# Performance work log

Hardware: AMD Instinct MI355X
Metric: run time of the kernel (lower is better)

## Reference

```python
import jax, jax.numpy as jnp
import numpy as np

B, FEAT, HID, LAT, NQ, NEMB = 2048, 840, 256, 128, 12, 512


def setup_inputs() -> dict:
    key = jax.random.key(0)
    ks = jax.random.split(key, 6)
    return {
        "x": jax.random.normal(ks[0], (B, FEAT), jnp.float32),
        "w1": jax.random.normal(ks[1], (HID, 1, 3), jnp.float32) * 0.1,   # Conv1d(1->256, k=3)
        "b1": jnp.zeros((HID,), jnp.float32),
        "w2": jax.random.normal(ks[2], (LAT, HID, 3), jnp.float32) * 0.05,  # Conv1d(256->128, k=3)
        "b2": jnp.zeros((LAT,), jnp.float32),
        # 12 codebooks of (512, 128), init uniform(-1/n_emb, 1/n_emb) per the torch code
        "codebooks": jax.random.uniform(ks[3], (NQ, NEMB, LAT), jnp.float32, -1.0 / NEMB, 1.0 / NEMB),
    }


def _encode(x, w1, b1, w2, b2):
    # x: (B, FEAT) -> unsqueeze channel dim -> NCW conv stack -> adaptive avg pool(1)
    h = x[:, None, :]  # (B, 1, FEAT)
    h = jax.lax.conv_general_dilated(h, w1, (1,), 'SAME',
                                     dimension_numbers=('NCH', 'OIH', 'NCH'))
    h = jax.nn.relu(h + b1[None, :, None])
    h = jax.lax.conv_general_dilated(h, w2, (1,), 'SAME',
                                     dimension_numbers=('NCH', 'OIH', 'NCH'))
    h = jax.nn.relu(h + b2[None, :, None])
    return h.mean(axis=2)  # AdaptiveAvgPool1d(1) + squeeze -> (B, LAT)


def _rvq(z_flat, codebooks):
    # sequential residual VQ: 12 stages of cdist -> argmin -> gather -> residual update
    def step(residual, cb):
        # squared L2 distances: ||r||^2 - 2 r C^T + ||c||^2, shape (B, NEMB)
        d = (jnp.sum(residual ** 2, axis=1, keepdims=True)
             - 2.0 * (residual @ cb.T)
             + jnp.sum(cb ** 2, axis=1)[None, :])
        idx = jnp.argmin(d, axis=1)          # (B,)
        q = cb[idx]                          # (B, LAT) embedding gather
        residual = residual - jax.lax.stop_gradient(q)  # .detach() in torch
        return residual, (q, idx)

    _, (qs, idxs) = jax.lax.scan(step, z_flat, codebooks)  # qs: (NQ, B, LAT)
    return qs.sum(axis=0), idxs.T  # (B, LAT), (B, NQ)


def reference(x, w1, b1, w2, b2, codebooks):
    z = _encode(x, w1, b1, w2, b2)            # (B, LAT)
    zq, idx = _rvq(z, codebooks)              # L = 1 so flat == (B, LAT)
    return zq[:, None, :], idx[:, None, :]    # (B, 1, LAT), (B, 1, NQ)
```

## Files before the change

### kernel.cpp

```cpp
#include <hip/hip_runtime.h>

#define B_SZ 2048
#define FEAT 840
#define HID  256
#define LAT  128
#define NQ   12
#define NEMB 512

#define T_SUB 40
#define NTILE 21
#define HSTR  46
#define H2STR 41
#define CHALF 128

__device__ __forceinline__ float np8_combine(const float* r) {
    float sA = __fadd_rn(r[0], r[1]);
    float sB = __fadd_rn(r[2], r[3]);
    float sC = __fadd_rn(r[4], r[5]);
    float sD = __fadd_rn(r[6], r[7]);
    return __fadd_rn(__fadd_rn(sA, sB), __fadd_rn(sC, sD));
}

__global__ __launch_bounds__(256) void w2r_kernel(const float* __restrict__ w2,
                                                  float* __restrict__ w2r)
{
    int p = blockIdx.x * 256 + threadIdx.x;
    if (p >= HID * 384) return;
    int c2 = p / 384, r = p - c2 * 384;
    int ly = r / 12, jk = r - ly * 12;
    int j = jk / 3, k = jk - j * 3;
    w2r[p] = w2[(size_t)(ly*4 + j)*768 + c2*3 + k];
}

template <int USE_WR>
__global__ __launch_bounds__(128) void enc_kernel(
    const float* __restrict__ x,  const float* __restrict__ w1,
    const float* __restrict__ b1, const float* __restrict__ w2,
    const float* __restrict__ w2r,
    const float* __restrict__ b2, float* __restrict__ zout)
{
    __shared__ float xp[FEAT + 4];
    __shared__ float h1s[CHALF * HSTR];
    __shared__ float leafs[LAT * 8];

    const int tid = threadIdx.x;
    const int b   = blockIdx.x;
    const int tx  = tid & 3;
    const int ly  = tid >> 2;
    const int u0  = tx * 10;

    const int ach = tid;
    float w1v[2][3], b1v[2];
#pragma unroll
    for (int hf = 0; hf < 2; ++hf) {
        int c = hf * CHALF + ach;
        w1v[hf][0] = w1[c*3 + 0];
        w1v[hf][1] = w1[c*3 + 1];
        w1v[hf][2] = w1[c*3 + 2];
        b1v[hf]    = b1[c];
    }
    float b2v[4];
#pragma unroll
    for (int j = 0; j < 4; ++j) b2v[j] = b2[ly*4 + j];

    for (int i = tid; i < FEAT + 2; i += 128)
        xp[i] = (i >= 1 && i <= FEAT) ? x[(size_t)b*FEAT + i - 1] : 0.f;

    float racc[8];
    int leaf_id = 0, leaf_pos = 0;
#pragma unroll
    for (int j = 0; j < 8; ++j) racc[j] = 0.f;

    __syncthreads();
    for (int t0 = 0; t0 < FEAT; t0 += T_SUB) {
        const bool edge = (t0 == 0) | (t0 + T_SUB == FEAT);

        float sk[4][10][3];
#pragma unroll
        for (int j = 0; j < 4; ++j)
#pragma unroll
            for (int i = 0; i < 10; ++i)
#pragma unroll
                for (int k = 0; k < 3; ++k) sk[j][i][k] = 0.f;

#pragma unroll
        for (int hf = 0; hf < 2; ++hf) {
            {
                const float wA = w1v[hf][0], wB = w1v[hf][1], wC = w1v[hf][2];
                const float bb = b1v[hf];
                if (edge) {
                    for (int tp = 0; tp < T_SUB + 2; ++tp) {
                        int tg = t0 - 1 + tp;
                        float v = 0.f;
                        if (tg >= 0 && tg < FEAT) {
                            float s = __fadd_rn(__fadd_rn(__fmul_rn(wA, xp[tg]),
                                                          __fmul_rn(wB, xp[tg+1])),
                                                __fmul_rn(wC, xp[tg+2]));
                            s = __fadd_rn(s, bb);
                            v = s > 0.f ? s : 0.f;
                        }
                        h1s[ach*HSTR + tp] = v;
                    }
                } else {
#pragma unroll 6
                    for (int tp = 0; tp < T_SUB + 2; ++tp) {
                        int tg = t0 - 1 + tp;
                        float s = __fadd_rn(__fadd_rn(__fmul_rn(wA, xp[tg]),
                                                      __fmul_rn(wB, xp[tg+1])),
                                            __fmul_rn(wC, xp[tg+2]));
                        s = __fadd_rn(s, bb);
                        h1s[ach*HSTR + tp] = s > 0.f ? s : 0.f;
                    }
                }
            }
            __syncthreads();

            if (USE_WR) {
                const float* __restrict__ wbase =
                    w2r + (size_t)(hf*CHALF)*384 + ly*12;
#pragma unroll 2
                for (int cc = 0; cc < CHALF; ++cc) {
                    const float4* __restrict__ wq =
                        (const float4*)(wbase + (size_t)cc*384);
                    float4 A0 = wq[0], A1 = wq[1], A2 = wq[2];
                    float w_[12];
                    w_[0]=A0.x; w_[1]=A0.y; w_[2]=A0.z; w_[3]=A0.w;
                    w_[4]=A1.x; w_[5]=A1.y; w_[6]=A1.z; w_[7]=A1.w;
                    w_[8]=A2.x; w_[9]=A2.y; w_[10]=A2.z; w_[11]=A2.w;

                    const float2* __restrict__ hq =
                        (const float2*)(&h1s[cc*HSTR + u0]);
                    float2 q0=hq[0], q1=hq[1], q2=hq[2], q3=hq[3], q4=hq[4], q5=hq[5];
                    float hv[12] = {q0.x,q0.y,q1.x,q1.y,q2.x,q2.y,
                                    q3.x,q3.y,q4.x,q4.y,q5.x,q5.y};
#pragma unroll
                    for (int j = 0; j < 4; ++j)
#pragma unroll
                        for (int i = 0; i < 10; ++i)
#pragma unroll
                            for (int k = 0; k < 3; ++k)
                                sk[j][i][k] = __fmaf_rn(w_[j*3+k], hv[i+k],
                                                        sk[j][i][k]);
                }
            } else {
                for (int cc = 0; cc < CHALF; ++cc) {
                    int c2 = hf*CHALF + cc;
                    const float* hp = &h1s[cc*HSTR + u0];
                    float hv[12];
#pragma unroll
                    for (int m = 0; m < 12; ++m) hv[m] = hp[m];
#pragma unroll
                    for (int j = 0; j < 4; ++j) {
                        float wa = w2[(size_t)(ly*4+j)*768 + c2*3 + 0];
                        float wb = w2[(size_t)(ly*4+j)*768 + c2*3 + 1];
                        float wc = w2[(size_t)(ly*4+j)*768 + c2*3 + 2];
#pragma unroll
                        for (int i = 0; i < 10; ++i) {
                            sk[j][i][0] = __fmaf_rn(wa, hv[i],   sk[j][i][0]);
                            sk[j][i][1] = __fmaf_rn(wb, hv[i+1], sk[j][i][1]);
                            sk[j][i][2] = __fmaf_rn(wc, hv[i+2], sk[j][i][2]);
                        }
                    }
                }
            }
            __syncthreads();
        }

#pragma unroll
        for (int j = 0; j < 4; ++j)
#pragma unroll
            for (int i = 0; i < 10; ++i) {
                float hh = __fadd_rn(__fadd_rn(sk[j][i][0], sk[j][i][1]), sk[j][i][2]);
                hh = __fadd_rn(hh, b2v[j]);
                hh = hh > 0.f ? hh : 0.f;
                h1s[(ly*4 + j)*H2STR + u0 + i] = hh;
            }
        __syncthreads();

        {
            for (int g = 0; g < T_SUB; g += 8) {
                float v[8];
#pragma unroll
                for (int m = 0; m < 8; ++m)
                    v[m] = h1s[tid*H2STR + g + m];
#pragma unroll
                for (int m = 0; m < 8; ++m) {
                    float vv = v[m];
                    int j = leaf_pos & 7;
                    racc[j] = (leaf_pos < 8) ? vv : __fadd_rn(racc[j], vv);
                    ++leaf_pos;
                    int llen = (leaf_id == 7) ? 112 : 104;
                    if (leaf_pos == llen) {
                        leafs[tid*8 + leaf_id] = np8_combine(racc);
                        ++leaf_id; leaf_pos = 0;
                    }
                }
            }
        }
        __syncthreads();
    }

    {
        const float* L = &leafs[tid*8];
        float s0 = __fadd_rn(L[0], L[1]);
        float s1 = __fadd_rn(L[2], L[3]);
        float sA = __fadd_rn(s0, s1);
        float s2 = __fadd_rn(L[4], L[5]);
        float s3 = __fadd_rn(L[6], L[7]);
        float sB = __fadd_rn(s2, s3);
        float tot = __fadd_rn(sA, sB);
        zout[(size_t)b*LAT + tid] = __fdiv_rn(tot, 840.0f);
    }
}

__global__ __launch_bounds__(256) void rvq32_kernel(
    const float* __restrict__ cb, const float* __restrict__ z,
    float* __restrict__ zqout, float* __restrict__ oidx)
{
    __shared__ float rr[LAT];
    __shared__ float Ash;
    __shared__ float redd[256];
    __shared__ int   rede[256];
    __shared__ float sredd[64];
    __shared__ int   srede[64];
    __shared__ int   beste;
    __shared__ float qv[NQ * LAT];

    const int tid = threadIdx.x;
    const int b   = blockIdx.x;

    if (tid < LAT) rr[tid] = z[(size_t)b*LAT + tid];
    __syncthreads();

    for (int q = 0; q < NQ; ++q) {
        const float* __restrict__ cbq = cb + (size_t)q * NEMB * LAT;

        if (tid == 0) {
            float r8[8];
#pragma unroll
            for (int j = 0; j < 8; ++j) r8[j] = __fmul_rn(rr[j], rr[j]);
            for (int i = 8; i < LAT; i += 8)
#pragma unroll
                for (int j = 0; j < 8; ++j)
                    r8[j] = __fadd_rn(r8[j], __fmul_rn(rr[i+j], rr[i+j]));
            Ash = np8_combine(r8);
        }
        __syncthreads();

        float dmin = 0.f; int emin = 0;
#pragma unroll
        for (int h = 0; h < 2; ++h) {
            int e = 2*tid + h;
            const float* __restrict__ cp = cbq + (size_t)e*LAT;
            float dot = 0.f;
            float c8[8];
#pragma unroll
            for (int j = 0; j < 8; ++j) {
                float c = cp[j];
                c8[j] = __fmul_rn(c, c);
                dot = __fmaf_rn(c, rr[j], dot);
            }
            for (int i = 8; i < LAT; i += 8)
#pragma unroll
                for (int j = 0; j < 8; ++j) {
                    float c = cp[i+j];
                    dot = __fmaf_rn(c, rr[i+j], dot);
                    c8[j] = __fadd_rn(c8[j], __fmul_rn(c, c));
                }
            float cn = np8_combine(c8);
            float G  = __fmul_rn(2.0f, dot);
            float d  = __fadd_rn(__fsub_rn(Ash, G), cn);
            if (h == 0) { dmin = d; emin = e; }
            else if (d < dmin) { dmin = d; emin = e; }
        }
        redd[tid] = dmin; rede[tid] = emin;
        __syncthreads();

        if (tid < 64) {
            float bb = redd[tid*4]; int ee = rede[tid*4];
            for (int j = 1; j < 4; ++j) {
                float dj = redd[tid*4 + j];
                if (dj < bb) { bb = dj; ee = rede[tid*4 + j]; }
            }
            sredd[tid] = bb; srede[tid] = ee;
        }
        __syncthreads();
        if (tid == 0) {
            float bb = sredd[0]; int ee = srede[0];
            for (int j = 1; j < 64; ++j) {
                float dj = sredd[j];
                if (dj < bb) { bb = dj; ee = srede[j]; }
            }
            beste = ee;
            oidx[(size_t)b*NQ + q] = (float)ee;
        }
        __syncthreads();

        if (tid < LAT) {
            float cv = cbq[(size_t)beste*LAT + tid];
            qv[q*LAT + tid] = cv;
            rr[tid] = __fsub_rn(rr[tid], cv);
        }
        __syncthreads();
    }

    if (tid < LAT) {
        float s = qv[tid];
        for (int s2 = 1; s2 < NQ; ++s2)
            s = __fadd_rn(s, qv[s2*LAT + tid]);
        zqout[(size_t)b*LAT + tid] = s;
    }
}

extern "C" void kernel_launch(void* const* d_in, const int* in_sizes, int n_in,
                              void* d_out, int out_size, void* d_ws, size_t ws_size,
                              hipStream_t stream)
{
    (void)in_sizes; (void)n_in; (void)out_size;
    const float* x  = (const float*)d_in[0];
    const float* w1 = (const float*)d_in[1];
    const float* b1 = (const float*)d_in[2];
    const float* w2 = (const float*)d_in[3];
    const float* b2 = (const float*)d_in[4];
    const float* cb = (const float*)d_in[5];

    float* out  = (float*)d_out;
    float* zq   = out;
    float* oidx = out + (size_t)B_SZ * LAT;

    const size_t w2r_bytes = (size_t)HID * 384 * sizeof(float);

    if (ws_size >= w2r_bytes) {
        float* w2r = (float*)d_ws;
        w2r_kernel<<<(HID*384 + 255)/256, 256, 0, stream>>>(w2, w2r);
        enc_kernel<1><<<B_SZ, 128, 0, stream>>>(x, w1, b1, w2, w2r, b2, zq);
    } else {
        enc_kernel<0><<<B_SZ, 128, 0, stream>>>(x, w1, b1, w2, nullptr, b2, zq);
    }
    rvq32_kernel<<<B_SZ, 256, 0, stream>>>(cb, zq, zq, oidx);
}
```

Measured before the change: 5.925 ms.

## Shrink encoder LDS to quarter-channel tiles and precompute codebook norms

The encoder now stages conv1 output in chunks of 64 channels instead of 128, with two threads per channel each computing half the time window. The conv2 writeback is split into two passes over a narrower buffer. Together these cut shared memory per block, which is meant to allow more resident blocks per CU, at the cost of extra barriers and w1 reloads from global memory. Separately, codebook squared norms are computed once in a new prepass kernel and read back in the RVQ kernel, removing the per-sample recomputation of 12×512 norms.

```diff
diff --git a/kernel.cpp b/kernel.cpp
--- a/kernel.cpp
+++ b/kernel.cpp
@@ -10,8 +10,12 @@
 #define T_SUB 40
 #define NTILE 21
 #define HSTR  46
-#define H2STR 41
-#define CHALF 128
+#define H2STR 21
+#define CQ    64
+#define HBUF  (CQ * HSTR)
+
+#define W2R_FLOATS ((size_t)HID * 384)
+#define CBN_FLOATS ((size_t)NQ * NEMB)
 
 __device__ __forceinline__ float np8_combine(const float* r) {
     float sA = __fadd_rn(r[0], r[1]);
@@ -32,6 +36,27 @@
     w2r[p] = w2[(size_t)(ly*4 + j)*768 + c2*3 + k];
 }
 
+__global__ __launch_bounds__(256) void cbn_kernel(const float* __restrict__ cb,
+                                                  float* __restrict__ cbn)
+{
+    int p = blockIdx.x * 256 + threadIdx.x;
+    if (p >= NQ * NEMB) return;
+    const float* __restrict__ cp = cb + (size_t)p * LAT;
+    float c8[8];
+#pragma unroll
+    for (int j = 0; j < 8; ++j) {
+        float c = cp[j];
+        c8[j] = __fmul_rn(c, c);
+    }
+    for (int i = 8; i < LAT; i += 8)
+#pragma unroll
+        for (int j = 0; j < 8; ++j) {
+            float c = cp[i+j];
+            c8[j] = __fadd_rn(c8[j], __fmul_rn(c, c));
+        }
+    cbn[p] = np8_combine(c8);
+}
+
 template <int USE_WR>
 __global__ __launch_bounds__(128) void enc_kernel(
     const float* __restrict__ x,  const float* __restrict__ w1,
@@ -40,7 +65,7 @@
     const float* __restrict__ b2, float* __restrict__ zout)
 {
     __shared__ float xp[FEAT + 4];
-    __shared__ float h1s[CHALF * HSTR];
+    __shared__ float h1s[HBUF];
     __shared__ float leafs[LAT * 8];
 
     const int tid = threadIdx.x;
@@ -49,16 +74,9 @@
     const int ly  = tid >> 2;
     const int u0  = tx * 10;
 
-    const int ach = tid;
-    float w1v[2][3], b1v[2];
-#pragma unroll
-    for (int hf = 0; hf < 2; ++hf) {
-        int c = hf * CHALF + ach;
-        w1v[hf][0] = w1[c*3 + 0];
-        w1v[hf][1] = w1[c*3 + 1];
-        w1v[hf][2] = w1[c*3 + 2];
-        b1v[hf]    = b1[c];
-    }
+    const int ach   = tid >> 1;
+    const int piece = tid & 1;
+
     float b2v[4];
 #pragma unroll
     for (int j = 0; j < 4; ++j) b2v[j] = b2[ly*4 + j];
@@ -83,13 +101,15 @@
 #pragma unroll
                 for (int k = 0; k < 3; ++k) sk[j][i][k] = 0.f;
 
-#pragma unroll
-        for (int hf = 0; hf < 2; ++hf) {
+#pragma unroll 1
+        for (int qf = 0; qf < 4; ++qf) {
             {
-                const float wA = w1v[hf][0], wB = w1v[hf][1], wC = w1v[hf][2];
-                const float bb = b1v[hf];
+                const int c = qf*CQ + ach;
+                const float wA = w1[c*3+0], wB = w1[c*3+1], wC = w1[c*3+2];
+                const float bb = b1[c];
+                const int tpb = piece * 21;
                 if (edge) {
-                    for (int tp = 0; tp < T_SUB + 2; ++tp) {
+                    for (int tp = tpb; tp < tpb + 21; ++tp) {
                         int tg = t0 - 1 + tp;
                         float v = 0.f;
                         if (tg >= 0 && tg < FEAT) {
@@ -102,8 +122,8 @@
                         h1s[ach*HSTR + tp] = v;
                     }
                 } else {
-#pragma unroll 6
-                    for (int tp = 0; tp < T_SUB + 2; ++tp) {
+#pragma unroll 7
+                    for (int tp = tpb; tp < tpb + 21; ++tp) {
                         int tg = t0 - 1 + tp;
                         float s = __fadd_rn(__fadd_rn(__fmul_rn(wA, xp[tg]),
                                                       __fmul_rn(wB, xp[tg+1])),
@@ -117,9 +137,9 @@
 
             if (USE_WR) {
                 const float* __restrict__ wbase =
-                    w2r + (size_t)(hf*CHALF)*384 + ly*12;
+                    w2r + (size_t)(qf*CQ)*384 + ly*12;
 #pragma unroll 2
-                for (int cc = 0; cc < CHALF; ++cc) {
+                for (int cc = 0; cc < CQ; ++cc) {
                     const float4* __restrict__ wq =
                         (const float4*)(wbase + (size_t)cc*384);
                     float4 A0 = wq[0], A1 = wq[1], A2 = wq[2];
@@ -143,8 +163,8 @@
                                                         sk[j][i][k]);
                 }
             } else {
-                for (int cc = 0; cc < CHALF; ++cc) {
-                    int c2 = hf*CHALF + cc;
+                for (int cc = 0; cc < CQ; ++cc) {
+                    int c2 = qf*CQ + cc;
                     const float* hp = &h1s[cc*HSTR + u0];
                     float hv[12];
 #pragma unroll
@@ -166,25 +186,29 @@
             __syncthreads();
         }
 
-#pragma unroll
-        for (int j = 0; j < 4; ++j)
-#pragma unroll
-            for (int i = 0; i < 10; ++i) {
-                float hh = __fadd_rn(__fadd_rn(sk[j][i][0], sk[j][i][1]), sk[j][i][2]);
-                hh = __fadd_rn(hh, b2v[j]);
-                hh = hh > 0.f ? hh : 0.f;
-                h1s[(ly*4 + j)*H2STR + u0 + i] = hh;
-            }
-        __syncthreads();
-
-        {
-            for (int g = 0; g < T_SUB; g += 8) {
-                float v[8];
-#pragma unroll
-                for (int m = 0; m < 8; ++m)
+#pragma unroll 1
+        for (int st = 0; st < 2; ++st) {
+            if ((tx >> 1) == st) {
+#pragma unroll
+                for (int j = 0; j < 4; ++j)
+#pragma unroll
+                    for (int i = 0; i < 10; ++i) {
+                        float hh = __fadd_rn(__fadd_rn(sk[j][i][0], sk[j][i][1]),
+                                             sk[j][i][2]);
+                        hh = __fadd_rn(hh, b2v[j]);
+                        hh = hh > 0.f ? hh : 0.f;
+                        h1s[(ly*4 + j)*H2STR + (u0 - st*20) + i] = hh;
+                    }
+            }
+            __syncthreads();
+
+            for (int g = 0; g < 20; g += 10) {
+                float v[10];
+#pragma unroll
+                for (int m = 0; m < 10; ++m)
                     v[m] = h1s[tid*H2STR + g + m];
 #pragma unroll
-                for (int m = 0; m < 8; ++m) {
+                for (int m = 0; m < 10; ++m) {
                     float vv = v[m];
                     int j = leaf_pos & 7;
                     racc[j] = (leaf_pos < 8) ? vv : __fadd_rn(racc[j], vv);
@@ -196,8 +220,8 @@
                     }
                 }
             }
-        }
-        __syncthreads();
+            __syncthreads();
+        }
     }
 
     {
@@ -213,8 +237,10 @@
     }
 }
 
+template <int USE_CN>
 __global__ __launch_bounds__(256) void rvq32_kernel(
-    const float* __restrict__ cb, const float* __restrict__ z,
+    const float* __restrict__ cb, const float* __restrict__ cbn,
+    const float* __restrict__ z,
     float* __restrict__ zqout, float* __restrict__ oidx)
 {
     __shared__ float rr[LAT];
@@ -253,21 +279,33 @@
             int e = 2*tid + h;
             const float* __restrict__ cp = cbq + (size_t)e*LAT;
             float dot = 0.f;
-            float c8[8];
-#pragma unroll
-            for (int j = 0; j < 8; ++j) {
-                float c = cp[j];
-                c8[j] = __fmul_rn(c, c);
-                dot = __fmaf_rn(c, rr[j], dot);
-            }
-            for (int i = 8; i < LAT; i += 8)
+            float cn;
+            if (USE_CN) {
+#pragma unroll
+                for (int j = 0; j < 8; ++j)
+                    dot = __fmaf_rn(cp[j], rr[j], dot);
+                for (int i = 8; i < LAT; i += 8)
+#pragma unroll
+                    for (int j = 0; j < 8; ++j)
+                        dot = __fmaf_rn(cp[i+j], rr[i+j], dot);
+                cn = cbn[(size_t)q*NEMB + e];
+            } else {
+                float c8[8];
 #pragma unroll
                 for (int j = 0; j < 8; ++j) {
-                    float c = cp[i+j];
-                    dot = __fmaf_rn(c, rr[i+j], dot);
-                    c8[j] = __fadd_rn(c8[j], __fmul_rn(c, c));
-                }
-            float cn = np8_combine(c8);
+                    float c = cp[j];
+                    c8[j] = __fmul_rn(c, c);
+                    dot = __fmaf_rn(c, rr[j], dot);
+                }
+                for (int i = 8; i < LAT; i += 8)
+#pragma unroll
+                    for (int j = 0; j < 8; ++j) {
+                        float c = cp[i+j];
+                        dot = __fmaf_rn(c, rr[i+j], dot);
+                        c8[j] = __fadd_rn(c8[j], __fmul_rn(c, c));
+                    }
+                cn = np8_combine(c8);
+            }
             float G  = __fmul_rn(2.0f, dot);
             float d  = __fadd_rn(__fsub_rn(Ash, G), cn);
             if (h == 0) { dmin = d; emin = e; }
@@ -328,14 +366,23 @@
     float* zq   = out;
     float* oidx = out + (size_t)B_SZ * LAT;
 
-    const size_t w2r_bytes = (size_t)HID * 384 * sizeof(float);
-
-    if (ws_size >= w2r_bytes) {
+    const size_t w2r_bytes  = W2R_FLOATS * sizeof(float);
+    const size_t full_bytes = (W2R_FLOATS + CBN_FLOATS) * sizeof(float);
+
+    if (ws_size >= full_bytes) {
+        float* w2r = (float*)d_ws;
+        float* cbn = (float*)d_ws + W2R_FLOATS;
+        w2r_kernel<<<(HID*384 + 255)/256, 256, 0, stream>>>(w2, w2r);
+        cbn_kernel<<<(NQ*NEMB + 255)/256, 256, 0, stream>>>(cb, cbn);
+        enc_kernel<1><<<B_SZ, 128, 0, stream>>>(x, w1, b1, w2, w2r, b2, zq);
+        rvq32_kernel<1><<<B_SZ, 256, 0, stream>>>(cb, cbn, zq, zq, oidx);
+    } else if (ws_size >= w2r_bytes) {
         float* w2r = (float*)d_ws;
         w2r_kernel<<<(HID*384 + 255)/256, 256, 0, stream>>>(w2, w2r);
         enc_kernel<1><<<B_SZ, 128, 0, stream>>>(x, w1, b1, w2, w2r, b2, zq);
+        rvq32_kernel<0><<<B_SZ, 256, 0, stream>>>(cb, nullptr, zq, zq, oidx);
     } else {
         enc_kernel<0><<<B_SZ, 128, 0, stream>>>(x, w1, b1, w2, nullptr, b2, zq);
-    }
-    rvq32_kernel<<<B_SZ, 256, 0, stream>>>(cb, zq, zq, oidx);
-}
+        rvq32_kernel<0><<<B_SZ, 256, 0, stream>>>(cb, nullptr, zq, zq, oidx);
+    }
+}
```

After: 5.517 ms. 6.9% less time.
